# Performance work log

Measured on AMD Instinct MI355X. Metric: run time of the kernel, lower is better.

Reference implementation:

```python
import jax, jax.numpy as jnp
import numpy as np
import math

D_MODEL = 512
HEAD_NUM = 8
HEAD_DIM = D_MODEL // HEAD_NUM


def setup_inputs() -> dict:
    key = jax.random.key(0)
    kq, kk, kv, km, k1, k2, k3, k4 = jax.random.split(key, 8)
    B, L = 4, 2048
    scale = 1.0 / math.sqrt(D_MODEL)
    return {
        "q": jax.random.normal(kq, (B, L, D_MODEL), dtype=jnp.float32),
        "k": jax.random.normal(kk, (B, L, D_MODEL), dtype=jnp.float32),
        "v": jax.random.normal(kv, (B, L, D_MODEL), dtype=jnp.float32),
        "mask": jax.random.randint(km, (B, L, L), 0, 2, dtype=jnp.int32),
        # Only q_linear and out are actually used in the source forward
        # (k_linear/v_linear are dead parameters -- preserved bug).
        "wq": jax.random.normal(k1, (D_MODEL, D_MODEL), dtype=jnp.float32) * scale,
        "bq": jax.random.normal(k2, (D_MODEL,), dtype=jnp.float32) * 0.02,
        "wo": jax.random.normal(k3, (D_MODEL, D_MODEL), dtype=jnp.float32) * scale,
        "bo": jax.random.normal(k4, (D_MODEL,), dtype=jnp.float32) * 0.02,
    }


def _split_head(x):
    # [B, L, D] -> [B, H, L, Dh]
    B, L, _ = x.shape
    return x.reshape(B, L, HEAD_NUM, HEAD_DIM).transpose(0, 2, 1, 3)


def reference(q, k, v, mask, wq, bq, wo, bo):
    # NOTE: source applies q_linear to q, k, and v (faithful to original bug)
    qp = _split_head(q @ wq.T + bq)
    kp = _split_head(k @ wq.T + bq)
    vp = _split_head(v @ wq.T + bq)
    # scores scaled by 1/sqrt(d_model) (as in source, not 1/sqrt(head_dim))
    scores = jnp.einsum("bhqd,bhkd->bhqk", qp, kp) / math.sqrt(D_MODEL)
    scores = jnp.where(mask[:, None, :, :] == 0, jnp.float32(-1e9), scores)
    attn = jax.nn.softmax(scores, axis=-1)
    ctx = jnp.einsum("bhqk,bhkd->bhqd", attn, vp)  # [B,H,L,Dh]
    B, _, L, _ = ctx.shape
    ctx = ctx.transpose(0, 2, 1, 3).reshape(B, L, D_MODEL)
    out = ctx @ wo.T + bo
    return out, attn
```

## Files before the change

kernel.cpp:

```cpp
#include <hip/hip_runtime.h>
#include <hip/hip_bf16.h>

#define L_SEQ 2048
#define DM 512
#define NH 8
#define DH 64
#define NB 4

typedef __attribute__((ext_vector_type(4))) float f32x4;
typedef __attribute__((ext_vector_type(8))) short bf16x8;
typedef __attribute__((ext_vector_type(4))) unsigned short u16x4;
typedef __attribute__((ext_vector_type(4))) int i32x4;
typedef unsigned long long u64;

__device__ __forceinline__ unsigned short f2bf(float f) {
  union { float f; unsigned u; } x; x.f = f;
  unsigned r = x.u + 0x7FFFu + ((x.u >> 16) & 1u);
  return (unsigned short)(r >> 16);
}

__global__ void pack_mask_k(const int* __restrict__ mask, u64* __restrict__ bits,
                            int nwords) {
  int lane = threadIdx.x & 63;
  int w0 = (blockIdx.x * blockDim.x + threadIdx.x) >> 6;
  int stride = (gridDim.x * blockDim.x) >> 6;
  for (int w = w0; w < nwords; w += stride) {
    int m = mask[(size_t)w * 64 + lane];
    u64 b = __ballot(m != 0);
    if (lane == 0) bits[w] = b;
  }
}

template<int MODE>
__global__ __launch_bounds__(256, 2)
void gemm_k(const void* __restrict__ A0, const void* __restrict__ A1,
            const void* __restrict__ A2, const float* __restrict__ Bw,
            const float* __restrict__ bias,
            void* __restrict__ O0, void* __restrict__ O1, void* __restrict__ O2) {
  __shared__ __align__(16) unsigned short As[128 * 64];
  __shared__ __align__(16) unsigned short Bs[128 * 64];
  const int tid = threadIdx.x;
  const int lane = tid & 63;
  const int wv = tid >> 6, wr = wv >> 1, wc = wv & 1;
  const int c = lane & 15, g = lane >> 4;
  const int m0 = blockIdx.x * 128, n0 = blockIdx.y * 128;
  const int z = blockIdx.z;
  const void* Ap = (z == 0) ? A0 : (z == 1) ? A1 : A2;
  void* Op = (z == 0) ? O0 : (z == 1) ? O1 : O2;

  f32x4 acc[4][4] = {};

  for (int kit = 0; kit < 8; ++kit) {
    const int k0 = kit * 64;
    if (kit) __syncthreads();
    if constexpr (MODE == 1) {
      const unsigned short* A = (const unsigned short*)Ap;
      #pragma unroll
      for (int f = 0; f < 4; ++f) {
        int p = tid + f * 256;
        int row = p >> 3, ch = p & 7;
        i32x4 vdat = *(const i32x4*)(A + (size_t)(m0 + row) * DM + k0 + ch * 8);
        *(i32x4*)(As + row * 64 + ((ch ^ (row & 7)) * 8)) = vdat;
      }
    } else {
      const float* A = (const float*)Ap;
      #pragma unroll
      for (int f = 0; f < 8; ++f) {
        int p = tid + f * 256;
        int row = p >> 4, c4 = p & 15;
        f32x4 vv = *(const f32x4*)(A + (size_t)(m0 + row) * DM + k0 + c4 * 4);
        u16x4 hh = { f2bf(vv[0]), f2bf(vv[1]), f2bf(vv[2]), f2bf(vv[3]) };
        int ch = c4 >> 1, half = c4 & 1;
        *(u16x4*)(As + row * 64 + ((ch ^ (row & 7)) * 8) + half * 4) = hh;
      }
    }
    #pragma unroll
    for (int f = 0; f < 8; ++f) {
      int p = tid + f * 256;
      int row = p >> 4, c4 = p & 15;
      f32x4 vv = *(const f32x4*)(Bw + (size_t)(n0 + row) * DM + k0 + c4 * 4);
      u16x4 hh = { f2bf(vv[0]), f2bf(vv[1]), f2bf(vv[2]), f2bf(vv[3]) };
      int ch = c4 >> 1, half = c4 & 1;
      *(u16x4*)(Bs + row * 64 + ((ch ^ (row & 7)) * 8) + half * 4) = hh;
    }
    __syncthreads();
    #pragma unroll
    for (int ks = 0; ks < 2; ++ks) {
      bf16x8 av[4], bv_[4];
      #pragma unroll
      for (int m = 0; m < 4; ++m) {
        int row = wr * 64 + m * 16 + c;
        av[m] = *(const bf16x8*)(As + row * 64 + (((ks * 4 + g) ^ (row & 7)) * 8));
      }
      #pragma unroll
      for (int n = 0; n < 4; ++n) {
        int row = wc * 64 + n * 16 + c;
        bv_[n] = *(const bf16x8*)(Bs + row * 64 + (((ks * 4 + g) ^ (row & 7)) * 8));
      }
      #pragma unroll
      for (int m = 0; m < 4; ++m)
        #pragma unroll
        for (int n = 0; n < 4; ++n)
          acc[m][n] = __builtin_amdgcn_mfma_f32_16x16x32_bf16(av[m], bv_[n], acc[m][n], 0, 0, 0);
    }
  }

  float bvx[4];
  #pragma unroll
  for (int n = 0; n < 4; ++n) bvx[n] = bias[n0 + wc * 64 + n * 16 + c];

  if constexpr (MODE == 0) {
    unsigned short* O = (unsigned short*)Op;
    if (z < 2) {
      #pragma unroll
      for (int n = 0; n < 4; ++n) {
        int j = n0 + wc * 64 + n * 16 + c;
        int hd = j >> 6, d = j & 63;
        #pragma unroll
        for (int m = 0; m < 4; ++m) {
          int ib = m0 + wr * 64 + m * 16 + g * 4;
          int bb = ib >> 11, tok = ib & (L_SEQ - 1);
          size_t base = (((size_t)(bb * NH + hd)) * L_SEQ + tok) * DH + d;
          #pragma unroll
          for (int r = 0; r < 4; ++r)
            O[base + (size_t)r * DH] = f2bf(acc[m][n][r] + bvx[n]);
        }
      }
    } else {
      #pragma unroll
      for (int n = 0; n < 4; ++n) {
        int j = n0 + wc * 64 + n * 16 + c;
        int hd = j >> 6, d = j & 63;
        #pragma unroll
        for (int m = 0; m < 4; ++m) {
          int ib = m0 + wr * 64 + m * 16 + g * 4;
          int bb = ib >> 11, tok = ib & (L_SEQ - 1);
          u16x4 hh = { f2bf(acc[m][n][0] + bvx[n]), f2bf(acc[m][n][1] + bvx[n]),
                       f2bf(acc[m][n][2] + bvx[n]), f2bf(acc[m][n][3] + bvx[n]) };
          *(u16x4*)(O + (((size_t)(bb * NH + hd)) * DH + d) * L_SEQ + tok) = hh;
        }
      }
    }
  } else {
    float* O = (float*)Op;
    #pragma unroll
    for (int n = 0; n < 4; ++n) {
      int j = n0 + wc * 64 + n * 16 + c;
      #pragma unroll
      for (int m = 0; m < 4; ++m) {
        int ib = m0 + wr * 64 + m * 16 + g * 4;
        #pragma unroll
        for (int r = 0; r < 4; ++r)
          O[(size_t)(ib + r) * DM + j] = acc[m][n][r] + bvx[n];
      }
    }
  }
}

__global__ __launch_bounds__(256, 2)
void attn_k(const unsigned short* __restrict__ qp,
            const unsigned short* __restrict__ kp,
            const unsigned short* __restrict__ vpT,
            const u64* __restrict__ mbits,
            float* __restrict__ attn,
            unsigned short* __restrict__ ctx) {
  __shared__ __align__(16) unsigned short Elds[2][64][128];
  __shared__ float rsl[2][128];
  const int tid = threadIdx.x;
  const int lane = tid & 63;
  const int wv = tid >> 6, wr = wv >> 1, wc = wv & 1;
  const int c = lane & 15, g = lane >> 4;
  const int bh = blockIdx.y, b = bh >> 3, hd = bh & 7;
  const int i0 = blockIdx.x * 128;
  const unsigned short* qb = qp + (size_t)bh * L_SEQ * DH;
  const unsigned short* kb = kp + (size_t)bh * L_SEQ * DH;
  const unsigned short* vb = vpT + (size_t)bh * DH * L_SEQ;
  float* ab = attn + (size_t)bh * L_SEQ * L_SEQ;
  const float SC = 0.044194173824159216f;

  bf16x8 qf[4][2];
  #pragma unroll
  for (int n = 0; n < 4; ++n)
    #pragma unroll
    for (int k = 0; k < 2; ++k)
      qf[n][k] = *(const bf16x8*)(qb + (size_t)(i0 + wc * 64 + n * 16 + c) * DH + k * 32 + g * 8);

  float rs[4] = {0.f, 0.f, 0.f, 0.f};

  for (int j0 = 0; j0 < L_SEQ; j0 += 128) {
    f32x4 acc[4][4] = {};
    #pragma unroll
    for (int k = 0; k < 2; ++k) {
      bf16x8 kf[4];
      #pragma unroll
      for (int m = 0; m < 4; ++m)
        kf[m] = *(const bf16x8*)(kb + (size_t)(j0 + wr * 64 + m * 16 + c) * DH + k * 32 + g * 8);
      #pragma unroll
      for (int m = 0; m < 4; ++m)
        #pragma unroll
        for (int n = 0; n < 4; ++n)
          acc[m][n] = __builtin_amdgcn_mfma_f32_16x16x32_bf16(kf[m], qf[n][k], acc[m][n], 0, 0, 0);
    }
    #pragma unroll
    for (int n = 0; n < 4; ++n) {
      int i = i0 + wc * 64 + n * 16 + c;
      u64 w = mbits[((size_t)b * L_SEQ + i) * (L_SEQ / 64) + (j0 >> 6) + wr];
      #pragma unroll
      for (int m = 0; m < 4; ++m)
        #pragma unroll
        for (int r = 0; r < 4; ++r) {
          float e = ((w >> (m * 16 + g * 4 + r)) & 1) ? __expf(acc[m][n][r] * SC) : 0.0f;
          rs[n] += e;
        }
    }
  }
  #pragma unroll
  for (int n = 0; n < 4; ++n) {
    rs[n] += __shfl_xor(rs[n], 16);
    rs[n] += __shfl_xor(rs[n], 32);
  }
  if (g == 0) {
    #pragma unroll
    for (int n = 0; n < 4; ++n) rsl[wr][wc * 64 + n * 16 + c] = rs[n];
  }
  __syncthreads();
  float inv[4];
  #pragma unroll
  for (int n = 0; n < 4; ++n) {
    int il = wc * 64 + n * 16 + c;
    inv[n] = 1.0f / (rsl[0][il] + rsl[1][il]);
  }

  f32x4 acc2[4][2] = {};
  const int wcE = wv >> 1;
  const int ilb = 32 * (wv & 1);

  for (int j0 = 0; j0 < L_SEQ; j0 += 128) {
    f32x4 acc[4][4] = {};
    #pragma unroll
    for (int k = 0; k < 2; ++k) {
      bf16x8 kf[4];
      #pragma unroll
      for (int m = 0; m < 4; ++m)
        kf[m] = *(const bf16x8*)(kb + (size_t)(j0 + wr * 64 + m * 16 + c) * DH + k * 32 + g * 8);
      #pragma unroll
      for (int m = 0; m < 4; ++m)
        #pragma unroll
        for (int n = 0; n < 4; ++n)
          acc[m][n] = __builtin_amdgcn_mfma_f32_16x16x32_bf16(kf[m], qf[n][k], acc[m][n], 0, 0, 0);
    }
    #pragma unroll
    for (int n = 0; n < 4; ++n) {
      int i = i0 + wc * 64 + n * 16 + c;
      u64 w = mbits[((size_t)b * L_SEQ + i) * (L_SEQ / 64) + (j0 >> 6) + wr];
      int il = n * 16 + c;
      #pragma unroll
      for (int m = 0; m < 4; ++m) {
        f32x4 fe;
        u16x4 he;
        #pragma unroll
        for (int r = 0; r < 4; ++r) {
          float e = ((w >> (m * 16 + g * 4 + r)) & 1) ? __expf(acc[m][n][r] * SC) : 0.0f;
          float val = e * inv[n];
          fe[r] = val;
          he[r] = f2bf(val);
        }
        *(f32x4*)(ab + (size_t)i * L_SEQ + j0 + wr * 64 + m * 16 + g * 4) = fe;
        int byteoff = (wr * 64 + m * 16 + g * 4) * 2;
        int fin = (byteoff & 15) | (((byteoff >> 4) ^ (il & 7)) << 4);
        *(u16x4*)((char*)(&Elds[wc][il][0]) + fin) = he;
      }
    }
    __syncthreads();
    #pragma unroll
    for (int ks = 0; ks < 4; ++ks) {
      bf16x8 ef[2];
      #pragma unroll
      for (int np = 0; np < 2; ++np) {
        int il = ilb + np * 16 + c;
        int fin = (((4 * ks + g) ^ (il & 7)) << 4);
        ef[np] = *(const bf16x8*)((const char*)(&Elds[wcE][il][0]) + fin);
      }
      bf16x8 vf[4];
      #pragma unroll
      for (int mp = 0; mp < 4; ++mp)
        vf[mp] = *(const bf16x8*)(vb + (size_t)(mp * 16 + c) * L_SEQ + j0 + ks * 32 + g * 8);
      #pragma unroll
      for (int mp = 0; mp < 4; ++mp)
        #pragma unroll
        for (int np = 0; np < 2; ++np)
          acc2[mp][np] = __builtin_amdgcn_mfma_f32_16x16x32_bf16(vf[mp], ef[np], acc2[mp][np], 0, 0, 0);
    }
    __syncthreads();
  }
  #pragma unroll
  for (int np = 0; np < 2; ++np) {
    int i = i0 + 32 * wv + np * 16 + c;
    size_t base = ((size_t)b * L_SEQ + i) * DM + hd * 64;
    #pragma unroll
    for (int mp = 0; mp < 4; ++mp) {
      u16x4 hh = { f2bf(acc2[mp][np][0]), f2bf(acc2[mp][np][1]),
                   f2bf(acc2[mp][np][2]), f2bf(acc2[mp][np][3]) };
      *(u16x4*)(ctx + base + mp * 16 + g * 4) = hh;
    }
  }
}

extern "C" void kernel_launch(void* const* d_in, const int* in_sizes, int n_in,
                              void* d_out, int out_size, void* d_ws, size_t ws_size,
                              hipStream_t stream) {
  const float* q    = (const float*)d_in[0];
  const float* k    = (const float*)d_in[1];
  const float* v    = (const float*)d_in[2];
  const int*   mask = (const int*)d_in[3];
  const float* wq   = (const float*)d_in[4];
  const float* bq   = (const float*)d_in[5];
  const float* wo   = (const float*)d_in[6];
  const float* bo   = (const float*)d_in[7];

  float* out  = (float*)d_out;
  float* attn = out + (size_t)NB * L_SEQ * DM;

  const size_t HEAD_ELEMS = (size_t)NB * NH * L_SEQ * DH;
  unsigned short* qp  = (unsigned short*)d_ws;
  unsigned short* kpb = qp + HEAD_ELEMS;
  unsigned short* vpT = kpb + HEAD_ELEMS;
  unsigned short* ctx = vpT + HEAD_ELEMS;
  u64* mbits = (u64*)(ctx + (size_t)NB * L_SEQ * DM);

  pack_mask_k<<<2048, 256, 0, stream>>>(mask, mbits, NB * L_SEQ * (L_SEQ / 64));

  dim3 gproj(64, 4, 3);
  gemm_k<0><<<gproj, 256, 0, stream>>>(q, k, v, wq, bq, qp, kpb, vpT);

  attn_k<<<dim3(L_SEQ / 128, NB * NH), 256, 0, stream>>>(qp, kpb, vpT, mbits, attn, ctx);

  dim3 gout(64, 4, 1);
  gemm_k<1><<<gout, 256, 0, stream>>>(ctx, nullptr, nullptr, wo, bo, out, nullptr, nullptr);
}
```

Measured before the change: 409.6 us.

## Double-buffer attention LDS, fold normalization into exp2, and prefetch V and mask

Double-buffers the probability LDS tile so each 128-column step needs one barrier instead of two. Softmax now uses exp2 with the log-sum folded into the exponent, which removes the per-element multiply by the inverse row sum. V fragments and mask words are prefetched before the exp stage, and the attn output uses nontemporal stores. It also adds MFMA priority hints, remaps blocks to spread heads across CUs, and swaps the bf16 conversion for the library intrinsic. The changes add register pressure and rely on fine-grained scheduling barriers.

```diff
diff --git a/kernel.cpp b/kernel.cpp
--- a/kernel.cpp
+++ b/kernel.cpp
@@ -14,9 +14,16 @@
 typedef unsigned long long u64;
 
 __device__ __forceinline__ unsigned short f2bf(float f) {
-  union { float f; unsigned u; } x; x.f = f;
-  unsigned r = x.u + 0x7FFFu + ((x.u >> 16) & 1u);
-  return (unsigned short)(r >> 16);
+  __hip_bfloat16 h = __float2bfloat16(f);
+  union { __hip_bfloat16 h; unsigned short u; } cv; cv.h = h; return cv.u;
+}
+
+__device__ __forceinline__ float fexp2(float x) {
+#if __has_builtin(__builtin_amdgcn_exp2f)
+  return __builtin_amdgcn_exp2f(x);
+#else
+  return __expf(x * 0.6931471805599453f);
+#endif
 }
 
 __global__ void pack_mask_k(const int* __restrict__ mask, u64* __restrict__ bits,
@@ -97,11 +104,13 @@
         int row = wc * 64 + n * 16 + c;
         bv_[n] = *(const bf16x8*)(Bs + row * 64 + (((ks * 4 + g) ^ (row & 7)) * 8));
       }
+      __builtin_amdgcn_s_setprio(1);
       #pragma unroll
       for (int m = 0; m < 4; ++m)
         #pragma unroll
         for (int n = 0; n < 4; ++n)
           acc[m][n] = __builtin_amdgcn_mfma_f32_16x16x32_bf16(av[m], bv_[n], acc[m][n], 0, 0, 0);
+      __builtin_amdgcn_s_setprio(0);
     }
   }
 
@@ -164,19 +173,23 @@
             const u64* __restrict__ mbits,
             float* __restrict__ attn,
             unsigned short* __restrict__ ctx) {
-  __shared__ __align__(16) unsigned short Elds[2][64][128];
+  __shared__ __align__(16) unsigned short Elds[2][2][64][128];
   __shared__ float rsl[2][128];
   const int tid = threadIdx.x;
   const int lane = tid & 63;
   const int wv = tid >> 6, wr = wv >> 1, wc = wv & 1;
   const int c = lane & 15, g = lane >> 4;
-  const int bh = blockIdx.y, b = bh >> 3, hd = bh & 7;
-  const int i0 = blockIdx.x * 128;
+  const int slot = blockIdx.x + blockIdx.y * gridDim.x;
+  const int work = (slot & 7) * 64 + (slot >> 3);
+  const int bh = work >> 4;
+  const int i0 = (work & 15) * 128;
+  const int b = bh >> 3;
   const unsigned short* qb = qp + (size_t)bh * L_SEQ * DH;
   const unsigned short* kb = kp + (size_t)bh * L_SEQ * DH;
   const unsigned short* vb = vpT + (size_t)bh * DH * L_SEQ;
   float* ab = attn + (size_t)bh * L_SEQ * L_SEQ;
-  const float SC = 0.044194173824159216f;
+  const float SCL2 = 0.044194173824159216f * 1.4426950408889634f;
+  const float NINF = -__builtin_inff();
 
   bf16x8 qf[4][2];
   #pragma unroll
@@ -195,23 +208,27 @@
       #pragma unroll
       for (int m = 0; m < 4; ++m)
         kf[m] = *(const bf16x8*)(kb + (size_t)(j0 + wr * 64 + m * 16 + c) * DH + k * 32 + g * 8);
+      __builtin_amdgcn_s_setprio(1);
       #pragma unroll
       for (int m = 0; m < 4; ++m)
         #pragma unroll
         for (int n = 0; n < 4; ++n)
           acc[m][n] = __builtin_amdgcn_mfma_f32_16x16x32_bf16(kf[m], qf[n][k], acc[m][n], 0, 0, 0);
+      __builtin_amdgcn_s_setprio(0);
     }
     #pragma unroll
     for (int n = 0; n < 4; ++n) {
       int i = i0 + wc * 64 + n * 16 + c;
       u64 w = mbits[((size_t)b * L_SEQ + i) * (L_SEQ / 64) + (j0 >> 6) + wr];
       #pragma unroll
-      for (int m = 0; m < 4; ++m)
+      for (int m = 0; m < 4; ++m) {
+        unsigned mw = (unsigned)(w >> (m * 16 + g * 4)) & 0xFu;
         #pragma unroll
         for (int r = 0; r < 4; ++r) {
-          float e = ((w >> (m * 16 + g * 4 + r)) & 1) ? __expf(acc[m][n][r] * SC) : 0.0f;
-          rs[n] += e;
-        }
+          float arg = ((mw >> r) & 1) ? acc[m][n][r] * SCL2 : NINF;
+          rs[n] += fexp2(arg);
+        }
+      }
     }
   }
   #pragma unroll
@@ -224,75 +241,101 @@
     for (int n = 0; n < 4; ++n) rsl[wr][wc * 64 + n * 16 + c] = rs[n];
   }
   __syncthreads();
-  float inv[4];
+  float l2i[4];
   #pragma unroll
   for (int n = 0; n < 4; ++n) {
     int il = wc * 64 + n * 16 + c;
-    inv[n] = 1.0f / (rsl[0][il] + rsl[1][il]);
+    l2i[n] = -__log2f(rsl[0][il] + rsl[1][il]);
   }
 
   f32x4 acc2[4][2] = {};
   const int wcE = wv >> 1;
   const int ilb = 32 * (wv & 1);
 
-  for (int j0 = 0; j0 < L_SEQ; j0 += 128) {
-    f32x4 acc[4][4] = {};
-    #pragma unroll
-    for (int k = 0; k < 2; ++k) {
-      bf16x8 kf[4];
-      #pragma unroll
-      for (int m = 0; m < 4; ++m)
-        kf[m] = *(const bf16x8*)(kb + (size_t)(j0 + wr * 64 + m * 16 + c) * DH + k * 32 + g * 8);
-      #pragma unroll
-      for (int m = 0; m < 4; ++m)
-        #pragma unroll
-        for (int n = 0; n < 4; ++n)
-          acc[m][n] = __builtin_amdgcn_mfma_f32_16x16x32_bf16(kf[m], qf[n][k], acc[m][n], 0, 0, 0);
-    }
-    #pragma unroll
-    for (int n = 0; n < 4; ++n) {
-      int i = i0 + wc * 64 + n * 16 + c;
-      u64 w = mbits[((size_t)b * L_SEQ + i) * (L_SEQ / 64) + (j0 >> 6) + wr];
-      int il = n * 16 + c;
-      #pragma unroll
-      for (int m = 0; m < 4; ++m) {
-        f32x4 fe;
-        u16x4 he;
-        #pragma unroll
-        for (int r = 0; r < 4; ++r) {
-          float e = ((w >> (m * 16 + g * 4 + r)) & 1) ? __expf(acc[m][n][r] * SC) : 0.0f;
-          float val = e * inv[n];
-          fe[r] = val;
-          he[r] = f2bf(val);
-        }
-        *(f32x4*)(ab + (size_t)i * L_SEQ + j0 + wr * 64 + m * 16 + g * 4) = fe;
-        int byteoff = (wr * 64 + m * 16 + g * 4) * 2;
-        int fin = (byteoff & 15) | (((byteoff >> 4) ^ (il & 7)) << 4);
-        *(u16x4*)((char*)(&Elds[wc][il][0]) + fin) = he;
-      }
-    }
-    __syncthreads();
-    #pragma unroll
-    for (int ks = 0; ks < 4; ++ks) {
-      bf16x8 ef[2];
-      #pragma unroll
-      for (int np = 0; np < 2; ++np) {
-        int il = ilb + np * 16 + c;
-        int fin = (((4 * ks + g) ^ (il & 7)) << 4);
-        ef[np] = *(const bf16x8*)((const char*)(&Elds[wcE][il][0]) + fin);
-      }
-      bf16x8 vf[4];
-      #pragma unroll
-      for (int mp = 0; mp < 4; ++mp)
-        vf[mp] = *(const bf16x8*)(vb + (size_t)(mp * 16 + c) * L_SEQ + j0 + ks * 32 + g * 8);
-      #pragma unroll
-      for (int mp = 0; mp < 4; ++mp)
-        #pragma unroll
-        for (int np = 0; np < 2; ++np)
-          acc2[mp][np] = __builtin_amdgcn_mfma_f32_16x16x32_bf16(vf[mp], ef[np], acc2[mp][np], 0, 0, 0);
-    }
-    __syncthreads();
-  }
+  for (int j0b = 0; j0b < L_SEQ; j0b += 256) {
+    #pragma unroll
+    for (int half = 0; half < 2; ++half) {
+      const int j0 = j0b + half * 128;
+      f32x4 acc[4][4] = {};
+      #pragma unroll
+      for (int k = 0; k < 2; ++k) {
+        bf16x8 kf[4];
+        #pragma unroll
+        for (int m = 0; m < 4; ++m)
+          kf[m] = *(const bf16x8*)(kb + (size_t)(j0 + wr * 64 + m * 16 + c) * DH + k * 32 + g * 8);
+        __builtin_amdgcn_s_setprio(1);
+        #pragma unroll
+        for (int m = 0; m < 4; ++m)
+          #pragma unroll
+          for (int n = 0; n < 4; ++n)
+            acc[m][n] = __builtin_amdgcn_mfma_f32_16x16x32_bf16(kf[m], qf[n][k], acc[m][n], 0, 0, 0);
+        __builtin_amdgcn_s_setprio(0);
+      }
+      bf16x8 vf01[2][4];
+      #pragma unroll
+      for (int ks = 0; ks < 2; ++ks)
+        #pragma unroll
+        for (int mp = 0; mp < 4; ++mp)
+          vf01[ks][mp] = *(const bf16x8*)(vb + (size_t)(mp * 16 + c) * L_SEQ + j0 + ks * 32 + g * 8);
+      u64 wm[4];
+      #pragma unroll
+      for (int n = 0; n < 4; ++n)
+        wm[n] = mbits[((size_t)b * L_SEQ + (i0 + wc * 64 + n * 16 + c)) * (L_SEQ / 64) + (j0 >> 6) + wr];
+      __builtin_amdgcn_sched_barrier(0);
+      #pragma unroll
+      for (int n = 0; n < 4; ++n) {
+        int i = i0 + wc * 64 + n * 16 + c;
+        int il = n * 16 + c;
+        #pragma unroll
+        for (int m = 0; m < 4; ++m) {
+          unsigned mw = (unsigned)(wm[n] >> (m * 16 + g * 4)) & 0xFu;
+          f32x4 fe;
+          u16x4 he;
+          #pragma unroll
+          for (int r = 0; r < 4; ++r) {
+            float arg = ((mw >> r) & 1) ? fmaf(acc[m][n][r], SCL2, l2i[n]) : NINF;
+            float val = fexp2(arg);
+            fe[r] = val;
+            he[r] = f2bf(val);
+          }
+          __builtin_nontemporal_store(fe, (f32x4*)(ab + (size_t)i * L_SEQ + j0 + wr * 64 + m * 16 + g * 4));
+          int byteoff = (wr * 64 + m * 16 + g * 4) * 2;
+          int fin = (byteoff & 15) | (((byteoff >> 4) ^ (il & 7)) << 4);
+          *(u16x4*)((char*)(&Elds[half][wc][il][0]) + fin) = he;
+        }
+      }
+      asm volatile("s_waitcnt lgkmcnt(0)" ::: "memory");
+      __builtin_amdgcn_sched_barrier(0);
+      __builtin_amdgcn_s_barrier();
+      __builtin_amdgcn_sched_barrier(0);
+      bf16x8 vf23[2][4];
+      #pragma unroll
+      for (int ks = 0; ks < 2; ++ks)
+        #pragma unroll
+        for (int mp = 0; mp < 4; ++mp)
+          vf23[ks][mp] = *(const bf16x8*)(vb + (size_t)(mp * 16 + c) * L_SEQ + j0 + (ks + 2) * 32 + g * 8);
+      __builtin_amdgcn_s_setprio(1);
+      #pragma unroll
+      for (int ks = 0; ks < 4; ++ks) {
+        bf16x8 ef[2];
+        #pragma unroll
+        for (int np = 0; np < 2; ++np) {
+          int il = ilb + np * 16 + c;
+          int fin = (((4 * ks + g) ^ (il & 7)) << 4);
+          ef[np] = *(const bf16x8*)((const char*)(&Elds[half][wcE][il][0]) + fin);
+        }
+        #pragma unroll
+        for (int mp = 0; mp < 4; ++mp) {
+          bf16x8 vfm = (ks < 2) ? vf01[ks][mp] : vf23[ks - 2][mp];
+          #pragma unroll
+          for (int np = 0; np < 2; ++np)
+            acc2[mp][np] = __builtin_amdgcn_mfma_f32_16x16x32_bf16(vfm, ef[np], acc2[mp][np], 0, 0, 0);
+        }
+      }
+      __builtin_amdgcn_s_setprio(0);
+    }
+  }
+  const int hd = bh & 7;
   #pragma unroll
   for (int np = 0; np < 2; ++np) {
     int i = i0 + 32 * wv + np * 16 + c;
```

New measurement: 328.6 us. 19.8% less time.

## Split attention into rowsum and fused softmax-PV kernels using exp2 and register shuffles

Applied to the files above, without the earlier changes.

Replaces the single two-pass attention kernel with a row-sum kernel that writes per-row -log2(sum) and a second kernel that folds normalization into exp2 via fma, so the per-element reciprocal multiply disappears. Each wave now owns 16 query rows, and probabilities reach the PV MFMA through ds_bpermute instead of an LDS tile with syncthreads. Attention stores are nontemporal, and both kernels use a remapped block order for locality. It also raises occupancy hints, adds setprio around MFMA blocks and switches to the library bf16 conversion. The cost is a third launch, recomputation of QK^T in both passes as before, and smaller per-wave reuse of K/V loads.

```diff
diff --git a/kernel.cpp b/kernel.cpp
--- a/kernel.cpp
+++ b/kernel.cpp
@@ -14,10 +14,19 @@
 typedef unsigned long long u64;
 
 __device__ __forceinline__ unsigned short f2bf(float f) {
-  union { float f; unsigned u; } x; x.f = f;
-  unsigned r = x.u + 0x7FFFu + ((x.u >> 16) & 1u);
-  return (unsigned short)(r >> 16);
-}
+  __hip_bfloat16 h = __float2bfloat16(f);
+  union { __hip_bfloat16 h; unsigned short u; } cv; cv.h = h; return cv.u;
+}
+
+__device__ __forceinline__ float fexp2(float x) {
+#if __has_builtin(__builtin_amdgcn_exp2f)
+  return __builtin_amdgcn_exp2f(x);
+#else
+  return __expf(x * 0.6931471805599453f);
+#endif
+}
+
+#define SCL2 (0.044194173824159216f * 1.4426950408889634f)
 
 __global__ void pack_mask_k(const int* __restrict__ mask, u64* __restrict__ bits,
                             int nwords) {
@@ -32,7 +41,7 @@
 }
 
 template<int MODE>
-__global__ __launch_bounds__(256, 2)
+__global__ __launch_bounds__(256, 3)
 void gemm_k(const void* __restrict__ A0, const void* __restrict__ A1,
             const void* __restrict__ A2, const float* __restrict__ Bw,
             const float* __restrict__ bias,
@@ -97,11 +106,13 @@
         int row = wc * 64 + n * 16 + c;
         bv_[n] = *(const bf16x8*)(Bs + row * 64 + (((ks * 4 + g) ^ (row & 7)) * 8));
       }
+      __builtin_amdgcn_s_setprio(1);
       #pragma unroll
       for (int m = 0; m < 4; ++m)
         #pragma unroll
         for (int n = 0; n < 4; ++n)
           acc[m][n] = __builtin_amdgcn_mfma_f32_16x16x32_bf16(av[m], bv_[n], acc[m][n], 0, 0, 0);
+      __builtin_amdgcn_s_setprio(0);
     }
   }
 
@@ -157,152 +168,160 @@
   }
 }
 
-__global__ __launch_bounds__(256, 2)
-void attn_k(const unsigned short* __restrict__ qp,
-            const unsigned short* __restrict__ kp,
-            const unsigned short* __restrict__ vpT,
-            const u64* __restrict__ mbits,
-            float* __restrict__ attn,
-            unsigned short* __restrict__ ctx) {
-  __shared__ __align__(16) unsigned short Elds[2][64][128];
-  __shared__ float rsl[2][128];
-  const int tid = threadIdx.x;
-  const int lane = tid & 63;
-  const int wv = tid >> 6, wr = wv >> 1, wc = wv & 1;
+__global__ __launch_bounds__(256, 4)
+void rowsum_k(const unsigned short* __restrict__ qp,
+              const unsigned short* __restrict__ kp,
+              const u64* __restrict__ mbits,
+              float* __restrict__ l2i) {
+  const int tid = threadIdx.x, lane = tid & 63;
+  const int wv = tid >> 6;
   const int c = lane & 15, g = lane >> 4;
-  const int bh = blockIdx.y, b = bh >> 3, hd = bh & 7;
-  const int i0 = blockIdx.x * 128;
+  const int slot = blockIdx.x + blockIdx.y * gridDim.x;
+  const int work = (slot & 7) * 128 + (slot >> 3);
+  const int bh = work >> 5;
+  const int i0 = (work & 31) * 64;
+  const int b = bh >> 3;
+  const unsigned short* qb = qp + (size_t)bh * L_SEQ * DH;
+  const unsigned short* kb = kp + (size_t)bh * L_SEQ * DH;
+  const int i = i0 + wv * 16 + c;
+  const float NINF = -__builtin_inff();
+
+  bf16x8 qf[2];
+  #pragma unroll
+  for (int k = 0; k < 2; ++k)
+    qf[k] = *(const bf16x8*)(qb + (size_t)i * DH + k * 32 + g * 8);
+  const int* mrow = (const int*)mbits + ((size_t)b * L_SEQ + i) * (L_SEQ / 32);
+
+  float rs = 0.0f;
+  for (int t = 0; t < 16; ++t) {
+    const int j0 = t * 128;
+    f32x4 acc[8] = {};
+    #pragma unroll
+    for (int k = 0; k < 2; ++k) {
+      bf16x8 kf[8];
+      #pragma unroll
+      for (int m = 0; m < 8; ++m)
+        kf[m] = *(const bf16x8*)(kb + (size_t)(j0 + m * 16 + c) * DH + k * 32 + g * 8);
+      __builtin_amdgcn_s_setprio(1);
+      #pragma unroll
+      for (int m = 0; m < 8; ++m)
+        acc[m] = __builtin_amdgcn_mfma_f32_16x16x32_bf16(kf[m], qf[k], acc[m], 0, 0, 0);
+      __builtin_amdgcn_s_setprio(0);
+    }
+    i32x4 mw = *(const i32x4*)(mrow + (j0 >> 5));
+    #pragma unroll
+    for (int m = 0; m < 8; ++m) {
+      unsigned bits4 = ((unsigned)mw[m >> 1] >> (((m & 1) * 16) + g * 4)) & 0xFu;
+      #pragma unroll
+      for (int r = 0; r < 4; ++r) {
+        float arg = ((bits4 >> r) & 1) ? acc[m][r] * SCL2 : NINF;
+        rs += fexp2(arg);
+      }
+    }
+  }
+  rs += __shfl_xor(rs, 16);
+  rs += __shfl_xor(rs, 32);
+  if (lane < 16)
+    l2i[(size_t)bh * L_SEQ + i0 + wv * 16 + lane] = -__log2f(rs);
+}
+
+__global__ __launch_bounds__(256, 3)
+void attnpv_k(const unsigned short* __restrict__ qp,
+              const unsigned short* __restrict__ kp,
+              const unsigned short* __restrict__ vpT,
+              const u64* __restrict__ mbits,
+              const float* __restrict__ l2i,
+              float* __restrict__ attn,
+              unsigned short* __restrict__ ctx) {
+  const int tid = threadIdx.x, lane = tid & 63;
+  const int wv = tid >> 6;
+  const int c = lane & 15, g = lane >> 4;
+  const int slot = blockIdx.x + blockIdx.y * gridDim.x;
+  const int work = (slot & 7) * 128 + (slot >> 3);
+  const int bh = work >> 5;
+  const int i0 = (work & 31) * 64;
+  const int b = bh >> 3, hd = bh & 7;
   const unsigned short* qb = qp + (size_t)bh * L_SEQ * DH;
   const unsigned short* kb = kp + (size_t)bh * L_SEQ * DH;
   const unsigned short* vb = vpT + (size_t)bh * DH * L_SEQ;
-  float* ab = attn + (size_t)bh * L_SEQ * L_SEQ;
-  const float SC = 0.044194173824159216f;
-
-  bf16x8 qf[4][2];
+  const int i = i0 + wv * 16 + c;
+  float* arow = attn + (size_t)bh * L_SEQ * L_SEQ + (size_t)i * L_SEQ;
+  const float NINF = -__builtin_inff();
+
+  bf16x8 qf[2];
   #pragma unroll
-  for (int n = 0; n < 4; ++n)
-    #pragma unroll
-    for (int k = 0; k < 2; ++k)
-      qf[n][k] = *(const bf16x8*)(qb + (size_t)(i0 + wc * 64 + n * 16 + c) * DH + k * 32 + g * 8);
-
-  float rs[4] = {0.f, 0.f, 0.f, 0.f};
-
-  for (int j0 = 0; j0 < L_SEQ; j0 += 128) {
-    f32x4 acc[4][4] = {};
+  for (int k = 0; k < 2; ++k)
+    qf[k] = *(const bf16x8*)(qb + (size_t)i * DH + k * 32 + g * 8);
+  const float li = l2i[(size_t)bh * L_SEQ + i];
+  const int* mrow = (const int*)mbits + ((size_t)b * L_SEQ + i) * (L_SEQ / 32);
+
+  const int idxA = 4 * (c + 16 * ((2 * g + 0) & 3));
+  const int idxB = 4 * (c + 16 * ((2 * g + 1) & 3));
+  const bool ghi = (g >= 2);
+
+  f32x4 acc2[4] = {};
+
+  for (int t = 0; t < 16; ++t) {
+    const int j0 = t * 128;
+    f32x4 acc[8] = {};
     #pragma unroll
     for (int k = 0; k < 2; ++k) {
-      bf16x8 kf[4];
-      #pragma unroll
-      for (int m = 0; m < 4; ++m)
-        kf[m] = *(const bf16x8*)(kb + (size_t)(j0 + wr * 64 + m * 16 + c) * DH + k * 32 + g * 8);
-      #pragma unroll
-      for (int m = 0; m < 4; ++m)
-        #pragma unroll
-        for (int n = 0; n < 4; ++n)
-          acc[m][n] = __builtin_amdgcn_mfma_f32_16x16x32_bf16(kf[m], qf[n][k], acc[m][n], 0, 0, 0);
-    }
-    #pragma unroll
-    for (int n = 0; n < 4; ++n) {
-      int i = i0 + wc * 64 + n * 16 + c;
-      u64 w = mbits[((size_t)b * L_SEQ + i) * (L_SEQ / 64) + (j0 >> 6) + wr];
-      #pragma unroll
-      for (int m = 0; m < 4; ++m)
-        #pragma unroll
-        for (int r = 0; r < 4; ++r) {
-          float e = ((w >> (m * 16 + g * 4 + r)) & 1) ? __expf(acc[m][n][r] * SC) : 0.0f;
-          rs[n] += e;
-        }
-    }
-  }
+      bf16x8 kf[8];
+      #pragma unroll
+      for (int m = 0; m < 8; ++m)
+        kf[m] = *(const bf16x8*)(kb + (size_t)(j0 + m * 16 + c) * DH + k * 32 + g * 8);
+      __builtin_amdgcn_s_setprio(1);
+      #pragma unroll
+      for (int m = 0; m < 8; ++m)
+        acc[m] = __builtin_amdgcn_mfma_f32_16x16x32_bf16(kf[m], qf[k], acc[m], 0, 0, 0);
+      __builtin_amdgcn_s_setprio(0);
+    }
+    i32x4 mw = *(const i32x4*)(mrow + (j0 >> 5));
+    int pk[8][2];
+    #pragma unroll
+    for (int m = 0; m < 8; ++m) {
+      unsigned bits4 = ((unsigned)mw[m >> 1] >> (((m & 1) * 16) + g * 4)) & 0xFu;
+      f32x4 fe;
+      #pragma unroll
+      for (int r = 0; r < 4; ++r) {
+        float arg = ((bits4 >> r) & 1) ? fmaf(acc[m][r], SCL2, li) : NINF;
+        fe[r] = fexp2(arg);
+      }
+      __builtin_nontemporal_store(fe, (f32x4*)(arow + j0 + m * 16 + g * 4));
+      pk[m][0] = (int)f2bf(fe[0]) | ((int)f2bf(fe[1]) << 16);
+      pk[m][1] = (int)f2bf(fe[2]) | ((int)f2bf(fe[3]) << 16);
+    }
+    bf16x8 vf[4][4];
+    #pragma unroll
+    for (int ks = 0; ks < 4; ++ks)
+      #pragma unroll
+      for (int dp = 0; dp < 4; ++dp)
+        vf[ks][dp] = *(const bf16x8*)(vb + (size_t)(dp * 16 + c) * L_SEQ + j0 + ks * 32 + g * 8);
+    #pragma unroll
+    for (int ks = 0; ks < 4; ++ks) {
+      int ew[4];
+      #pragma unroll
+      for (int q = 0; q < 4; ++q) {
+        int idx = (q < 2) ? idxA : idxB;
+        int va = __builtin_amdgcn_ds_bpermute(idx, pk[2 * ks][q & 1]);
+        int vb2 = __builtin_amdgcn_ds_bpermute(idx, pk[2 * ks + 1][q & 1]);
+        ew[q] = ghi ? vb2 : va;
+      }
+      union { i32x4 w; bf16x8 h; } ef;
+      ef.w = (i32x4){ew[0], ew[1], ew[2], ew[3]};
+      __builtin_amdgcn_s_setprio(1);
+      #pragma unroll
+      for (int dp = 0; dp < 4; ++dp)
+        acc2[dp] = __builtin_amdgcn_mfma_f32_16x16x32_bf16(vf[ks][dp], ef.h, acc2[dp], 0, 0, 0);
+      __builtin_amdgcn_s_setprio(0);
+    }
+  }
+  size_t cbase = ((size_t)b * L_SEQ + i) * DM + hd * 64;
   #pragma unroll
-  for (int n = 0; n < 4; ++n) {
-    rs[n] += __shfl_xor(rs[n], 16);
-    rs[n] += __shfl_xor(rs[n], 32);
-  }
-  if (g == 0) {
-    #pragma unroll
-    for (int n = 0; n < 4; ++n) rsl[wr][wc * 64 + n * 16 + c] = rs[n];
-  }
-  __syncthreads();
-  float inv[4];
-  #pragma unroll
-  for (int n = 0; n < 4; ++n) {
-    int il = wc * 64 + n * 16 + c;
-    inv[n] = 1.0f / (rsl[0][il] + rsl[1][il]);
-  }
-
-  f32x4 acc2[4][2] = {};
-  const int wcE = wv >> 1;
-  const int ilb = 32 * (wv & 1);
-
-  for (int j0 = 0; j0 < L_SEQ; j0 += 128) {
-    f32x4 acc[4][4] = {};
-    #pragma unroll
-    for (int k = 0; k < 2; ++k) {
-      bf16x8 kf[4];
-      #pragma unroll
-      for (int m = 0; m < 4; ++m)
-        kf[m] = *(const bf16x8*)(kb + (size_t)(j0 + wr * 64 + m * 16 + c) * DH + k * 32 + g * 8);
-      #pragma unroll
-      for (int m = 0; m < 4; ++m)
-        #pragma unroll
-        for (int n = 0; n < 4; ++n)
-          acc[m][n] = __builtin_amdgcn_mfma_f32_16x16x32_bf16(kf[m], qf[n][k], acc[m][n], 0, 0, 0);
-    }
-    #pragma unroll
-    for (int n = 0; n < 4; ++n) {
-      int i = i0 + wc * 64 + n * 16 + c;
-      u64 w = mbits[((size_t)b * L_SEQ + i) * (L_SEQ / 64) + (j0 >> 6) + wr];
-      int il = n * 16 + c;
-      #pragma unroll
-      for (int m = 0; m < 4; ++m) {
-        f32x4 fe;
-        u16x4 he;
-        #pragma unroll
-        for (int r = 0; r < 4; ++r) {
-          float e = ((w >> (m * 16 + g * 4 + r)) & 1) ? __expf(acc[m][n][r] * SC) : 0.0f;
-          float val = e * inv[n];
-          fe[r] = val;
-          he[r] = f2bf(val);
-        }
-        *(f32x4*)(ab + (size_t)i * L_SEQ + j0 + wr * 64 + m * 16 + g * 4) = fe;
-        int byteoff = (wr * 64 + m * 16 + g * 4) * 2;
-        int fin = (byteoff & 15) | (((byteoff >> 4) ^ (il & 7)) << 4);
-        *(u16x4*)((char*)(&Elds[wc][il][0]) + fin) = he;
-      }
-    }
-    __syncthreads();
-    #pragma unroll
-    for (int ks = 0; ks < 4; ++ks) {
-      bf16x8 ef[2];
-      #pragma unroll
-      for (int np = 0; np < 2; ++np) {
-        int il = ilb + np * 16 + c;
-        int fin = (((4 * ks + g) ^ (il & 7)) << 4);
-        ef[np] = *(const bf16x8*)((const char*)(&Elds[wcE][il][0]) + fin);
-      }
-      bf16x8 vf[4];
-      #pragma unroll
-      for (int mp = 0; mp < 4; ++mp)
-        vf[mp] = *(const bf16x8*)(vb + (size_t)(mp * 16 + c) * L_SEQ + j0 + ks * 32 + g * 8);
-      #pragma unroll
-      for (int mp = 0; mp < 4; ++mp)
-        #pragma unroll
-        for (int np = 0; np < 2; ++np)
-          acc2[mp][np] = __builtin_amdgcn_mfma_f32_16x16x32_bf16(vf[mp], ef[np], acc2[mp][np], 0, 0, 0);
-    }
-    __syncthreads();
-  }
-  #pragma unroll
-  for (int np = 0; np < 2; ++np) {
-    int i = i0 + 32 * wv + np * 16 + c;
-    size_t base = ((size_t)b * L_SEQ + i) * DM + hd * 64;
-    #pragma unroll
-    for (int mp = 0; mp < 4; ++mp) {
-      u16x4 hh = { f2bf(acc2[mp][np][0]), f2bf(acc2[mp][np][1]),
-                   f2bf(acc2[mp][np][2]), f2bf(acc2[mp][np][3]) };
-      *(u16x4*)(ctx + base + mp * 16 + g * 4) = hh;
-    }
+  for (int dp = 0; dp < 4; ++dp) {
+    u16x4 hh = { f2bf(acc2[dp][0]), f2bf(acc2[dp][1]),
+                 f2bf(acc2[dp][2]), f2bf(acc2[dp][3]) };
+    *(u16x4*)(ctx + cbase + dp * 16 + g * 4) = hh;
   }
 }
 
@@ -327,13 +346,16 @@
   unsigned short* vpT = kpb + HEAD_ELEMS;
   unsigned short* ctx = vpT + HEAD_ELEMS;
   u64* mbits = (u64*)(ctx + (size_t)NB * L_SEQ * DM);
+  float* l2i = (float*)(mbits + (size_t)NB * L_SEQ * (L_SEQ / 64));
 
   pack_mask_k<<<2048, 256, 0, stream>>>(mask, mbits, NB * L_SEQ * (L_SEQ / 64));
 
   dim3 gproj(64, 4, 3);
   gemm_k<0><<<gproj, 256, 0, stream>>>(q, k, v, wq, bq, qp, kpb, vpT);
 
-  attn_k<<<dim3(L_SEQ / 128, NB * NH), 256, 0, stream>>>(qp, kpb, vpT, mbits, attn, ctx);
+  rowsum_k<<<dim3(32, 32), 256, 0, stream>>>(qp, kpb, mbits, l2i);
+
+  attnpv_k<<<dim3(32, 32), 256, 0, stream>>>(qp, kpb, vpT, mbits, l2i, attn, ctx);
 
   dim3 gout(64, 4, 1);
   gemm_k<1><<<gout, 256, 0, stream>>>(ctx, nullptr, nullptr, wo, bo, out, nullptr, nullptr);
```

Result: slower. 466.9 us (+14.0%).
